# Optimization experiments

Measured on AMD Instinct MI355X. Metric: run time of the kernel, lower is better.

## Reference

```python
import jax, jax.numpy as jnp
import numpy as np

TEMPERATURE = 0.1

def setup_inputs() -> dict:
    key = jax.random.key(0)
    k1, k2 = jax.random.split(key)
    z_i = jax.random.normal(k1, (4096, 128), dtype=jnp.float32)
    z_j = jax.random.normal(k2, (4096, 128), dtype=jnp.float32)
    return {"z_i": z_i, "z_j": z_j}

def reference(z_i, z_j):
    n = z_i.shape[0]
    reps = jnp.concatenate([z_i, z_j], axis=0)              # (2N, D)
    # cosine similarity via normalize + GEMM (same math as broadcasted CosineSimilarity,
    # torch eps=1e-8 on the norm)
    norms = jnp.maximum(jnp.linalg.norm(reps, axis=1, keepdims=True), 1e-8)
    rn = reps / norms
    sim = rn @ rn.T                                          # (2N, 2N)
    l_pos = jnp.diagonal(sim, offset=n)                      # (N,)
    r_pos = jnp.diagonal(sim, offset=-n)                     # (N,)
    positives = jnp.concatenate([l_pos, r_pos])[:, None]     # (2N, 1)
    # NOTE: original code's mask bug makes `negatives` the FULL sim matrix
    logits = jnp.concatenate([positives, sim], axis=1) / TEMPERATURE  # (2N, 2N+1)
    # cross-entropy with label 0, reduction='sum'
    log_probs = jax.nn.log_softmax(logits, axis=1)
    loss = -jnp.sum(log_probs[:, 0])
    return loss / (2 * n)
```

## Files before the change

kernel.cpp:

```cpp
#include <hip/hip_runtime.h>
#include <hip/hip_bf16.h>

typedef __bf16 bf16x8 __attribute__((ext_vector_type(8)));
typedef __bf16 bf16x2 __attribute__((ext_vector_type(2)));
typedef float f32x4 __attribute__((ext_vector_type(4)));

#define NROWS 8192
#define HALF_N 4096
#define DIM 128
#define ROW_BYTES 256
#define TINV 10.0f
#define C1 14.42695040888963f
#define LN2 0.6931471805599453f
#define COL_SPLITS 8
#define COLS_PER (NROWS / COL_SPLITS)
#define ITERS (COLS_PER / 128)
#define NBLOCKS (COL_SPLITS * (NROWS / 128))

#define SWZ(r, kc) ((kc) ^ ((r) & 7))

__global__ __launch_bounds__(256) void k_normalize(
    const float* __restrict__ zi, const float* __restrict__ zj,
    char* __restrict__ rn, float* __restrict__ rowsum,
    unsigned int* __restrict__ done)
{
    const int wv   = threadIdx.x >> 6;
    const int lane = threadIdx.x & 63;
    #pragma unroll
    for (int i = 0; i < 4; ++i) {
        const int row = blockIdx.x * 16 + wv * 4 + i;
        const float* src = (row < HALF_N) ? (zi + (size_t)row * DIM)
                                          : (zj + (size_t)(row - HALF_N) * DIM);
        float2 v = *(const float2*)(src + lane * 2);
        float ss = v.x * v.x + v.y * v.y;
        #pragma unroll
        for (int m = 32; m >= 1; m >>= 1) ss += __shfl_xor(ss, m, 64);
        const float scale = 1.0f / fmaxf(sqrtf(ss), 1e-8f);
        bf16x2 o; o[0] = (__bf16)(v.x * scale); o[1] = (__bf16)(v.y * scale);
        char* dst = rn + (size_t)row * ROW_BYTES + SWZ(row, lane >> 2) * 16 + (lane & 3) * 4;
        *(bf16x2*)dst = o;
    }
    if (blockIdx.x < 32) rowsum[blockIdx.x * 256 + threadIdx.x] = 0.0f;
    if (blockIdx.x == 0 && threadIdx.x == 0) *done = 0u;
}

__global__ __launch_bounds__(256) void k_simsum(
    const char* __restrict__ rn, float* __restrict__ rowsum,
    float* __restrict__ pbuf, unsigned int* __restrict__ done,
    float* __restrict__ out)
{
    __shared__ char lds[2][128 * ROW_BYTES];
    const int tid  = threadIdx.x;
    const int wave = tid >> 6;
    const int lane = tid & 63;
    const int tile_m = blockIdx.x * 128;
    const int w0 = wave & 1, w1 = wave >> 1;
    const int qrow = lane >> 4;
    const int lcol = lane & 15;
    const int col_base = blockIdx.y * COLS_PER;
    const int prel = (((tile_m + HALF_N) & (NROWS - 1)) - col_base);
    const int it_p = (prel >= 0 && prel < COLS_PER) ? (prel >> 7) : -1;

    auto stage = [&](int it2, int pp) {
        const char* g = rn + (size_t)(col_base + it2 * 128) * ROW_BYTES;
        #pragma unroll
        for (int i = 0; i < 8; ++i) {
            const int off = wave * 8192 + i * 1024;
            __builtin_amdgcn_global_load_lds(
                (const __attribute__((address_space(1))) void*)(g + off + lane * 16),
                (__attribute__((address_space(3))) void*)(&lds[pp][off]),
                16, 0, 0);
        }
    };

    stage(0, 0);

    bf16x8 afrag[4][4];
    #pragma unroll
    for (int mi = 0; mi < 4; ++mi) {
        const int m = tile_m + w1 * 64 + mi * 16 + lcol;
        #pragma unroll
        for (int ks = 0; ks < 4; ++ks)
            afrag[mi][ks] = *(const bf16x8*)(rn + (size_t)m * ROW_BYTES
                                             + SWZ(m, ks * 4 + qrow) * 16);
    }

    stage(1, 1);

    float rsum[4][4];
    #pragma unroll
    for (int mi = 0; mi < 4; ++mi)
        #pragma unroll
        for (int r = 0; r < 4; ++r) rsum[mi][r] = 0.0f;

    #pragma unroll 1
    for (int it = 0; it < ITERS; ++it) {
        const int p = it & 1;
        if (it == ITERS - 1)
            asm volatile("s_waitcnt vmcnt(0)\n\ts_barrier" ::: "memory");
        else
            asm volatile("s_waitcnt vmcnt(8)\n\ts_barrier" ::: "memory");

        f32x4 acc[4][4];
        const f32x4 zero = {0.0f, 0.0f, 0.0f, 0.0f};
        #pragma unroll
        for (int mi = 0; mi < 4; ++mi)
            #pragma unroll
            for (int ni = 0; ni < 4; ++ni) acc[mi][ni] = zero;

        #pragma unroll
        for (int ks = 0; ks < 4; ++ks) {
            bf16x8 bfrag[4];
            #pragma unroll
            for (int ni = 0; ni < 4; ++ni) {
                const int n = w0 * 64 + ni * 16 + lcol;
                bfrag[ni] = *(const bf16x8*)(&lds[p][n * ROW_BYTES
                                             + SWZ(n, ks * 4 + qrow) * 16]);
            }
            #pragma unroll
            for (int mi = 0; mi < 4; ++mi)
                #pragma unroll
                for (int ni = 0; ni < 4; ++ni)
                    acc[mi][ni] = __builtin_amdgcn_mfma_f32_16x16x32_bf16(
                        afrag[mi][ks], bfrag[ni], acc[mi][ni], 0, 0, 0);
        }

        asm volatile("s_barrier" ::: "memory");
        if (it + 2 < ITERS) stage(it + 2, p);

        if (it == it_p) {
            #pragma unroll
            for (int mi = 0; mi < 4; ++mi) {
                const int rl = w1 * 64 + mi * 16 + qrow * 4;
                #pragma unroll
                for (int ni = 0; ni < 4; ++ni) {
                    const int cl = w0 * 64 + ni * 16 + lcol;
                    #pragma unroll
                    for (int rr = 0; rr < 4; ++rr)
                        if (cl == rl + rr)
                            __hip_atomic_store(&pbuf[tile_m + rl + rr], acc[mi][ni][rr],
                                               __ATOMIC_RELAXED, __HIP_MEMORY_SCOPE_AGENT);
                }
            }
        }

        #pragma unroll
        for (int mi = 0; mi < 4; ++mi)
            #pragma unroll
            for (int ni = 0; ni < 4; ++ni)
                #pragma unroll
                for (int r = 0; r < 4; ++r)
                    rsum[mi][r] += __builtin_amdgcn_exp2f(acc[mi][ni][r] * C1 - C1);
    }

    #pragma unroll
    for (int mi = 0; mi < 4; ++mi)
        #pragma unroll
        for (int r = 0; r < 4; ++r) {
            float v = rsum[mi][r];
            v += __shfl_xor(v, 1, 64);
            v += __shfl_xor(v, 2, 64);
            v += __shfl_xor(v, 4, 64);
            v += __shfl_xor(v, 8, 64);
            if (lcol == 0)
                atomicAdd(&rowsum[tile_m + w1 * 64 + mi * 16 + qrow * 4 + r], v);
        }

    __syncthreads();
    __shared__ int is_last;
    if (tid == 0) {
        __threadfence();
        unsigned old = __hip_atomic_fetch_add(done, 1u, __ATOMIC_ACQ_REL,
                                              __HIP_MEMORY_SCOPE_AGENT);
        is_last = (old == NBLOCKS - 1);
    }
    __syncthreads();
    if (!is_last) return;
    __threadfence();

    float lsum = 0.0f;
    for (int r = tid; r < NROWS; r += 256) {
        float rs = __hip_atomic_load(&rowsum[r], __ATOMIC_RELAXED, __HIP_MEMORY_SCOPE_AGENT);
        float pv = __hip_atomic_load(&pbuf[r],   __ATOMIC_RELAXED, __HIP_MEMORY_SCOPE_AGENT);
        float S  = rs + __builtin_amdgcn_exp2f(pv * C1 - C1);
        lsum += TINV + __builtin_amdgcn_logf(S) * LN2 - TINV * pv;
    }
    #pragma unroll
    for (int m = 32; m >= 1; m >>= 1) lsum += __shfl_xor(lsum, m, 64);
    __shared__ float part[4];
    if (lane == 0) part[wave] = lsum;
    __syncthreads();
    if (tid == 0)
        out[0] = (part[0] + part[1] + part[2] + part[3]) * (1.0f / (float)NROWS);
}

extern "C" void kernel_launch(void* const* d_in, const int* in_sizes, int n_in,
                              void* d_out, int out_size, void* d_ws, size_t ws_size,
                              hipStream_t stream)
{
    const float* zi = (const float*)d_in[0];
    const float* zj = (const float*)d_in[1];
    float* out = (float*)d_out;

    char*  rn     = (char*)d_ws;
    float* rowsum = (float*)((char*)d_ws + (size_t)NROWS * ROW_BYTES);
    float* pbuf   = rowsum + NROWS;
    unsigned int* done = (unsigned int*)(pbuf + NROWS);

    k_normalize<<<NROWS / 16, 256, 0, stream>>>(zi, zj, rn, rowsum, done);
    k_simsum<<<dim3(NROWS / 128, COL_SPLITS), 256, 0, stream>>>(rn, rowsum, pbuf, done, out);
}
```

Baseline: 104.8 us.

## Fuse normalize and similarity-sum kernels with per-block readiness flags

Merges the normalize and simsum kernels into one persistent-style launch of 512 blocks. Each block normalizes its own 16 rows, publishes a flag, then spin-waits only on the flags of the row and column blocks it needs before running the GEMM and exp-sum. The A operand is stored pre-scaled by 1/(T·ln2) so the exp2 argument needs no extra FMA, and the log-sum-exp shift is dropped. It also halves the LDS stage width and targets two blocks per CU. This adds a memset launch and inter-block spin-waiting, which assumes all blocks can be co-resident. Dropping the max shift relies on cosine values being bounded so exp2 cannot overflow.

```diff
diff --git a/kernel.cpp b/kernel.cpp
--- a/kernel.cpp
+++ b/kernel.cpp
@@ -2,90 +2,102 @@
 #include <hip/hip_bf16.h>
 
 typedef __bf16 bf16x8 __attribute__((ext_vector_type(8)));
-typedef __bf16 bf16x2 __attribute__((ext_vector_type(2)));
 typedef float f32x4 __attribute__((ext_vector_type(4)));
 
 #define NROWS 8192
 #define HALF_N 4096
 #define DIM 128
 #define ROW_BYTES 256
-#define TINV 10.0f
 #define C1 14.42695040888963f
 #define LN2 0.6931471805599453f
-#define COL_SPLITS 8
-#define COLS_PER (NROWS / COL_SPLITS)
-#define ITERS (COLS_PER / 128)
-#define NBLOCKS (COL_SPLITS * (NROWS / 128))
+#define NBLK 512
+#define CS_COLS 1024
+#define STAGE_COLS 64
+#define ITERS 16
 
 #define SWZ(r, kc) ((kc) ^ ((r) & 7))
 
-__global__ __launch_bounds__(256) void k_normalize(
+__global__ __launch_bounds__(256, 2) void k_fused(
     const float* __restrict__ zi, const float* __restrict__ zj,
-    char* __restrict__ rn, float* __restrict__ rowsum,
-    unsigned int* __restrict__ done)
+    char* __restrict__ rn, char* __restrict__ rnA,
+    float* __restrict__ rowsum, float* __restrict__ pbuf,
+    unsigned int* __restrict__ flag, unsigned int* __restrict__ done,
+    float* __restrict__ out)
 {
-    const int wv   = threadIdx.x >> 6;
-    const int lane = threadIdx.x & 63;
+    __shared__ char lds_b[2][STAGE_COLS * ROW_BYTES];
+    const int tid  = threadIdx.x;
+    const int wave = tid >> 6;
+    const int lane = tid & 63;
+    const int rg = blockIdx.x >> 3;
+    const int cs = blockIdx.x & 7;
+    const int w0 = wave & 1, w1 = wave >> 1;
+    const int qrow = lane >> 4, lcol = lane & 15;
+
     #pragma unroll
     for (int i = 0; i < 4; ++i) {
-        const int row = blockIdx.x * 16 + wv * 4 + i;
+        const int row = blockIdx.x * 16 + wave * 4 + i;
         const float* src = (row < HALF_N) ? (zi + (size_t)row * DIM)
                                           : (zj + (size_t)(row - HALF_N) * DIM);
         float2 v = *(const float2*)(src + lane * 2);
         float ss = v.x * v.x + v.y * v.y;
         #pragma unroll
         for (int m = 32; m >= 1; m >>= 1) ss += __shfl_xor(ss, m, 64);
-        const float scale = 1.0f / fmaxf(sqrtf(ss), 1e-8f);
-        bf16x2 o; o[0] = (__bf16)(v.x * scale); o[1] = (__bf16)(v.y * scale);
-        char* dst = rn + (size_t)row * ROW_BYTES + SWZ(row, lane >> 2) * 16 + (lane & 3) * 4;
-        *(bf16x2*)dst = o;
-    }
-    if (blockIdx.x < 32) rowsum[blockIdx.x * 256 + threadIdx.x] = 0.0f;
-    if (blockIdx.x == 0 && threadIdx.x == 0) *done = 0u;
-}
-
-__global__ __launch_bounds__(256) void k_simsum(
-    const char* __restrict__ rn, float* __restrict__ rowsum,
-    float* __restrict__ pbuf, unsigned int* __restrict__ done,
-    float* __restrict__ out)
-{
-    __shared__ char lds[2][128 * ROW_BYTES];
-    const int tid  = threadIdx.x;
-    const int wave = tid >> 6;
-    const int lane = tid & 63;
-    const int tile_m = blockIdx.x * 128;
-    const int w0 = wave & 1, w1 = wave >> 1;
-    const int qrow = lane >> 4;
-    const int lcol = lane & 15;
-    const int col_base = blockIdx.y * COLS_PER;
-    const int prel = (((tile_m + HALF_N) & (NROWS - 1)) - col_base);
-    const int it_p = (prel >= 0 && prel < COLS_PER) ? (prel >> 7) : -1;
-
-    auto stage = [&](int it2, int pp) {
-        const char* g = rn + (size_t)(col_base + it2 * 128) * ROW_BYTES;
-        #pragma unroll
-        for (int i = 0; i < 8; ++i) {
-            const int off = wave * 8192 + i * 1024;
+        const float sc = 1.0f / fmaxf(sqrtf(ss), 1e-8f);
+        union { __bf16 h[2]; unsigned u; } a, b;
+        a.h[0] = (__bf16)(v.x * sc);      a.h[1] = (__bf16)(v.y * sc);
+        b.h[0] = (__bf16)(v.x * sc * C1); b.h[1] = (__bf16)(v.y * sc * C1);
+        const size_t off = (size_t)row * ROW_BYTES + SWZ(row, lane >> 2) * 16 + (lane & 3) * 4;
+        __hip_atomic_store((unsigned*)(rn  + off), a.u, __ATOMIC_RELAXED, __HIP_MEMORY_SCOPE_AGENT);
+        __hip_atomic_store((unsigned*)(rnA + off), b.u, __ATOMIC_RELAXED, __HIP_MEMORY_SCOPE_AGENT);
+    }
+    if (tid < 16)
+        __hip_atomic_store((unsigned*)&rowsum[blockIdx.x * 16 + tid], 0u,
+                           __ATOMIC_RELAXED, __HIP_MEMORY_SCOPE_AGENT);
+    __syncthreads();
+    if (tid == 0)
+        __hip_atomic_store(&flag[blockIdx.x], 1u, __ATOMIC_RELEASE, __HIP_MEMORY_SCOPE_AGENT);
+
+    {
+        const unsigned* fA = &flag[rg * 8 + (lane & 7)];
+        const unsigned* fB = &flag[cs * 64 + lane];
+        int spins = 0;
+        for (;;) {
+            unsigned a = __hip_atomic_load(fA, __ATOMIC_ACQUIRE, __HIP_MEMORY_SCOPE_AGENT);
+            unsigned b = __hip_atomic_load(fB, __ATOMIC_ACQUIRE, __HIP_MEMORY_SCOPE_AGENT);
+            if (__ballot(a && b) == ~0ull) break;
+            __builtin_amdgcn_s_sleep(8);
+            if (++spins > (1 << 20)) break;
+        }
+        __threadfence();
+    }
+
+    auto stage_b = [&](int s) {
+        const char* g = rn + ((size_t)cs * CS_COLS + s * STAGE_COLS) * ROW_BYTES;
+        #pragma unroll
+        for (int i = 0; i < 4; ++i) {
+            const int off = wave * 4096 + i * 1024;
             __builtin_amdgcn_global_load_lds(
                 (const __attribute__((address_space(1))) void*)(g + off + lane * 16),
-                (__attribute__((address_space(3))) void*)(&lds[pp][off]),
+                (__attribute__((address_space(3))) void*)(&lds_b[s & 1][off]),
                 16, 0, 0);
         }
     };
 
-    stage(0, 0);
-
+    stage_b(0);
     bf16x8 afrag[4][4];
     #pragma unroll
     for (int mi = 0; mi < 4; ++mi) {
-        const int m = tile_m + w1 * 64 + mi * 16 + lcol;
+        const int m = rg * 128 + w1 * 64 + mi * 16 + lcol;
         #pragma unroll
         for (int ks = 0; ks < 4; ++ks)
-            afrag[mi][ks] = *(const bf16x8*)(rn + (size_t)m * ROW_BYTES
+            afrag[mi][ks] = *(const bf16x8*)(rnA + (size_t)m * ROW_BYTES
                                              + SWZ(m, ks * 4 + qrow) * 16);
     }
-
-    stage(1, 1);
+    stage_b(1);
+
+    const int pcol0 = (rg * 128 + HALF_N) & (NROWS - 1);
+    const int s_p = (pcol0 >= cs * CS_COLS && pcol0 < cs * CS_COLS + CS_COLS)
+                        ? (pcol0 - cs * CS_COLS) / STAGE_COLS : -999;
 
     float rsum[4][4];
     #pragma unroll
@@ -95,51 +107,50 @@
 
     #pragma unroll 1
     for (int it = 0; it < ITERS; ++it) {
-        const int p = it & 1;
         if (it == ITERS - 1)
             asm volatile("s_waitcnt vmcnt(0)\n\ts_barrier" ::: "memory");
         else
-            asm volatile("s_waitcnt vmcnt(8)\n\ts_barrier" ::: "memory");
-
-        f32x4 acc[4][4];
+            asm volatile("s_waitcnt vmcnt(4)\n\ts_barrier" ::: "memory");
+
+        f32x4 acc[4][2];
         const f32x4 zero = {0.0f, 0.0f, 0.0f, 0.0f};
         #pragma unroll
-        for (int mi = 0; mi < 4; ++mi)
+        for (int mi = 0; mi < 4; ++mi) { acc[mi][0] = zero; acc[mi][1] = zero; }
+
+        #pragma unroll
+        for (int ks = 0; ks < 4; ++ks) {
+            bf16x8 bfrag[2];
             #pragma unroll
-            for (int ni = 0; ni < 4; ++ni) acc[mi][ni] = zero;
-
-        #pragma unroll
-        for (int ks = 0; ks < 4; ++ks) {
-            bf16x8 bfrag[4];
-            #pragma unroll
-            for (int ni = 0; ni < 4; ++ni) {
-                const int n = w0 * 64 + ni * 16 + lcol;
-                bfrag[ni] = *(const bf16x8*)(&lds[p][n * ROW_BYTES
+            for (int ni = 0; ni < 2; ++ni) {
+                const int n = w0 * 32 + ni * 16 + lcol;
+                bfrag[ni] = *(const bf16x8*)(&lds_b[it & 1][n * ROW_BYTES
                                              + SWZ(n, ks * 4 + qrow) * 16]);
             }
             #pragma unroll
             for (int mi = 0; mi < 4; ++mi)
                 #pragma unroll
-                for (int ni = 0; ni < 4; ++ni)
+                for (int ni = 0; ni < 2; ++ni)
                     acc[mi][ni] = __builtin_amdgcn_mfma_f32_16x16x32_bf16(
                         afrag[mi][ks], bfrag[ni], acc[mi][ni], 0, 0, 0);
         }
 
         asm volatile("s_barrier" ::: "memory");
-        if (it + 2 < ITERS) stage(it + 2, p);
-
-        if (it == it_p) {
-            #pragma unroll
-            for (int mi = 0; mi < 4; ++mi) {
-                const int rl = w1 * 64 + mi * 16 + qrow * 4;
+        if (it + 2 < ITERS) stage_b(it + 2);
+
+        if (it == s_p || it == s_p + 1) {
+            const int h = it - s_p;
+            if (w1 == h) {
                 #pragma unroll
-                for (int ni = 0; ni < 4; ++ni) {
-                    const int cl = w0 * 64 + ni * 16 + lcol;
+                for (int mi = 0; mi < 4; ++mi) {
+                    const int o64 = mi * 16 + qrow * 4;
                     #pragma unroll
-                    for (int rr = 0; rr < 4; ++rr)
-                        if (cl == rl + rr)
-                            __hip_atomic_store(&pbuf[tile_m + rl + rr], acc[mi][ni][rr],
-                                               __ATOMIC_RELAXED, __HIP_MEMORY_SCOPE_AGENT);
+                    for (int ni = 0; ni < 2; ++ni)
+                        #pragma unroll
+                        for (int rr = 0; rr < 4; ++rr)
+                            if (o64 + rr == w0 * 32 + ni * 16 + lcol)
+                                __hip_atomic_store(&pbuf[rg * 128 + h * 64 + o64 + rr],
+                                                   acc[mi][ni][rr],
+                                                   __ATOMIC_RELAXED, __HIP_MEMORY_SCOPE_AGENT);
                 }
             }
         }
@@ -147,10 +158,10 @@
         #pragma unroll
         for (int mi = 0; mi < 4; ++mi)
             #pragma unroll
-            for (int ni = 0; ni < 4; ++ni)
+            for (int ni = 0; ni < 2; ++ni)
                 #pragma unroll
                 for (int r = 0; r < 4; ++r)
-                    rsum[mi][r] += __builtin_amdgcn_exp2f(acc[mi][ni][r] * C1 - C1);
+                    rsum[mi][r] += __builtin_amdgcn_exp2f(acc[mi][ni][r]);
     }
 
     #pragma unroll
@@ -163,7 +174,7 @@
             v += __shfl_xor(v, 4, 64);
             v += __shfl_xor(v, 8, 64);
             if (lcol == 0)
-                atomicAdd(&rowsum[tile_m + w1 * 64 + mi * 16 + qrow * 4 + r], v);
+                atomicAdd(&rowsum[rg * 128 + w1 * 64 + mi * 16 + qrow * 4 + r], v);
         }
 
     __syncthreads();
@@ -172,7 +183,7 @@
         __threadfence();
         unsigned old = __hip_atomic_fetch_add(done, 1u, __ATOMIC_ACQ_REL,
                                               __HIP_MEMORY_SCOPE_AGENT);
-        is_last = (old == NBLOCKS - 1);
+        is_last = (old == NBLK - 1);
     }
     __syncthreads();
     if (!is_last) return;
@@ -182,8 +193,8 @@
     for (int r = tid; r < NROWS; r += 256) {
         float rs = __hip_atomic_load(&rowsum[r], __ATOMIC_RELAXED, __HIP_MEMORY_SCOPE_AGENT);
         float pv = __hip_atomic_load(&pbuf[r],   __ATOMIC_RELAXED, __HIP_MEMORY_SCOPE_AGENT);
-        float S  = rs + __builtin_amdgcn_exp2f(pv * C1 - C1);
-        lsum += TINV + __builtin_amdgcn_logf(S) * LN2 - TINV * pv;
+        float S  = rs + __builtin_amdgcn_exp2f(pv);
+        lsum += (__builtin_amdgcn_logf(S) - pv) * LN2;
     }
     #pragma unroll
     for (int m = 32; m >= 1; m >>= 1) lsum += __shfl_xor(lsum, m, 64);
@@ -203,10 +214,12 @@
     float* out = (float*)d_out;
 
     char*  rn     = (char*)d_ws;
-    float* rowsum = (float*)((char*)d_ws + (size_t)NROWS * ROW_BYTES);
+    char*  rnA    = rn + (size_t)NROWS * ROW_BYTES;
+    float* rowsum = (float*)(rnA + (size_t)NROWS * ROW_BYTES);
     float* pbuf   = rowsum + NROWS;
-    unsigned int* done = (unsigned int*)(pbuf + NROWS);
-
-    k_normalize<<<NROWS / 16, 256, 0, stream>>>(zi, zj, rn, rowsum, done);
-    k_simsum<<<dim3(NROWS / 128, COL_SPLITS), 256, 0, stream>>>(rn, rowsum, pbuf, done, out);
+    unsigned int* flag = (unsigned int*)(pbuf + NROWS);
+    unsigned int* done = flag + NBLK;
+
+    hipMemsetAsync(flag, 0, (NBLK + 1) * sizeof(unsigned int), stream);
+    k_fused<<<NBLK, 256, 0, stream>>>(zi, zj, rn, rnA, rowsum, pbuf, flag, done, out);
 }
```

Result: slower. 210.1 us (+100.5%).
